# Kernel optimization log

Measured on AMD Instinct MI355X. Metric: run time of the kernel, lower is better.

The kernel has to match this reference:

```python
import jax, jax.numpy as jnp
import numpy as np
from jax import lax

B, T, E = 256, 128, 768      # batch, seq_len, bert emb dim
HE = 256                     # encoder lstm hidden (per direction)
H = 512                      # decoder hidden = 2*HE
SLOT, INTENT = 120, 64
EMB = SLOT // 3              # 40
V = SLOT + 1                 # 121, bos id = SLOT
DIN = EMB + 2 * H            # 1064 decoder lstm input
NEG = -1e12


def lstm_cell(x, h, c, Wih, Whh, bih, bhh):
    # torch gate order: i, f, g, o
    g = x @ Wih.T + h @ Whh.T + (bih + bhh)
    i, f, gg, o = jnp.split(g, 4, axis=-1)
    c = jax.nn.sigmoid(f) * c + jax.nn.sigmoid(i) * jnp.tanh(gg)
    h = jax.nn.sigmoid(o) * jnp.tanh(c)
    return h, c


def setup_inputs() -> dict:
    key = jax.random.key(0)
    ks = jax.random.split(key, 24)
    s = 0.05
    n = lambda k, shp: jax.random.normal(k, shp, jnp.float32) * s
    return {
        'seq_reps': jax.random.normal(ks[0], (B, T, E), jnp.float32),
        'nwp_index': jax.random.randint(ks[1], (B, T, 1), 0, 2),
        'slot_output_mask': jax.random.randint(ks[2], (B, T), 0, 2).astype(bool),
        'emb_table': jax.random.uniform(ks[3], (V, EMB), jnp.float32, -0.1, 0.1),
        # encoder fwd / bwd LSTM
        'Wf_ih': n(ks[4], (4 * HE, E)), 'Wf_hh': n(ks[5], (4 * HE, HE)),
        'bf_ih': n(ks[6], (4 * HE,)), 'bf_hh': n(ks[7], (4 * HE,)),
        'Wb_ih': n(ks[8], (4 * HE, E)), 'Wb_hh': n(ks[9], (4 * HE, HE)),
        'bb_ih': n(ks[10], (4 * HE,)), 'bb_hh': n(ks[11], (4 * HE,)),
        # decoder LSTM
        'Wd_ih': n(ks[12], (4 * H, DIN)), 'Wd_hh': n(ks[13], (4 * H, H)),
        'bd_ih': n(ks[14], (4 * H,)), 'bd_hh': n(ks[15], (4 * H,)),
        # attention + output heads
        'attn_W': n(ks[16], (H, H)), 'attn_b': n(ks[17], (H,)),
        'slot_W': n(ks[18], (SLOT, 2 * H)), 'slot_b': n(ks[19], (SLOT,)),
        'intent_W': n(ks[20], (INTENT, 2 * H)), 'intent_b': n(ks[21], (INTENT,)),
    }


def forward(seq_reps, nwp_index, slot_output_mask, emb_table,
            Wf_ih, Wf_hh, bf_ih, bf_hh, Wb_ih, Wb_hh, bb_ih, bb_hh,
            Wd_ih, Wd_hh, bd_ih, bd_hh, attn_W, attn_b,
            slot_W, slot_b, intent_W, intent_b):
    # ---------- Encoder: 1-layer bidirectional LSTM ----------
    xs = seq_reps.transpose(1, 0, 2)  # [T,B,E]
    z = jnp.zeros((B, HE), seq_reps.dtype)

    def fstep(carry, x):
        h, c = lstm_cell(x, carry[0], carry[1], Wf_ih, Wf_hh, bf_ih, bf_hh)
        return (h, c), h

    def bstep(carry, x):
        h, c = lstm_cell(x, carry[0], carry[1], Wb_ih, Wb_hh, bb_ih, bb_hh)
        return (h, c), h

    _, hf = lax.scan(fstep, (z, z), xs)
    _, hb = lax.scan(bstep, (z, z), xs[::-1])
    enc = jnp.concatenate([hf, hb[::-1]], -1).transpose(1, 0, 2)  # [B,T,512]

    # last real hidden: out[b, #nonzero(nwp_index[b])]
    count = jnp.clip((nwp_index[:, :, 0] != 0).sum(1), 0, T - 1)
    last_hidden = enc[jnp.arange(B), count]  # [B,H]

    # ---------- Attention (energies independent of step -> precompute) ----------
    energies = enc @ attn_W.T + attn_b  # [B,T,H]

    def attention(h):  # h: [B,H]
        e = jnp.einsum('bth,bh->bt', energies, h)
        e = jnp.where(slot_output_mask, NEG, e)
        alpha = jax.nn.softmax(e, -1)
        return jnp.einsum('bt,bth->bh', alpha, enc)  # [B,H]

    # ---------- Decoder: per-timestep LSTM + attention ----------
    bos_emb = jnp.broadcast_to(emb_table[SLOT], (B, EMB))
    zH = jnp.zeros((B, H), seq_reps.dtype)
    aligns = enc.transpose(1, 0, 2)  # [T,B,H]

    def dstep(carry, aligned):
        emb, ctx, h, c = carry
        inp = jnp.concatenate([emb, ctx, aligned], -1)  # [B,1064]
        h, c = lstm_cell(inp, h, c, Wd_ih, Wd_hh, bd_ih, bd_hh)
        score = jnp.concatenate([h, ctx], -1) @ slot_W.T + slot_b
        logp = jax.nn.log_softmax(score, -1)
        nxt = jnp.argmax(logp, -1)
        emb = emb_table[nxt]
        ctx_new = attention(h)
        return (emb, ctx_new, h, c), (logp, h, ctx_new)

    _, (logps, h_seq, ctx_seq) = lax.scan(dstep, (bos_emb, last_hidden, zH, zH), aligns)

    slot_scores = logps.transpose(1, 0, 2)  # [B,T,SLOT]
    # intent computed at step 0: intent_context == attention(h after step 0) == ctx_seq[0]
    intent_score = jnp.concatenate([h_seq[0], ctx_seq[0]], -1) @ intent_W.T + intent_b
    return slot_scores, intent_score


def reference(seq_reps, nwp_index, slot_output_mask, emb_table,
              Wf_ih, Wf_hh, bf_ih, bf_hh, Wb_ih, Wb_hh, bb_ih, bb_hh,
              Wd_ih, Wd_hh, bd_ih, bd_hh, attn_W, attn_b,
              slot_W, slot_b, intent_W, intent_b):
    return forward(seq_reps, nwp_index, slot_output_mask, emb_table,
                   Wf_ih, Wf_hh, bf_ih, bf_hh, Wb_ih, Wb_hh, bb_ih, bb_hh,
                   Wd_ih, Wd_hh, bd_ih, bd_hh, attn_W, attn_b,
                   slot_W, slot_b, intent_W, intent_b)
```

## Files before the change

### kernel.cpp

```cpp
#include <hip/hip_runtime.h>
#include <math.h>

#define Bn 256
#define Tn 128
#define En 768
#define HEn 256
#define Hn 512
#define SLOTn 120
#define INTENTn 64
#define EMBn 40
#define NEGV -1e12f

__device__ __forceinline__ float sigm(float x) { return 1.0f / (1.0f + expf(-x)); }

__global__ void zero_k(float* __restrict__ p, int n) {
    int i = blockIdx.x * blockDim.x + threadIdx.x;
    int stride = gridDim.x * blockDim.x;
    for (; i < n; i += stride) p[i] = 0.f;
}

__global__ void detect_mask_k(const unsigned char* __restrict__ m, int* __restrict__ flag) {
    __shared__ int any;
    if (threadIdx.x == 0) any = 0;
    __syncthreads();
    int found = 0;
    for (int i = threadIdx.x; i < 32768; i += 256) {
        if ((i & 3) != 0 && m[i] != 0) found = 1;
    }
    if (found) atomicOr(&any, 1);
    __syncthreads();
    if (threadIdx.x == 0) *flag = any;
}

__global__ __launch_bounds__(256) void slotwt_k(const float* __restrict__ W,
                                               float* __restrict__ wT4) {
    int idx = blockIdx.x * 256 + threadIdx.x;
    int k = idx >> 7, s = idx & 127;
    float v = (s < SLOTn) ? W[(size_t)s * 1024 + k] : 0.f;
    wT4[((size_t)(k >> 2) * 128 + s) * 4 + (k & 3)] = v;
}

__device__ __forceinline__ float4 f4zero() { float4 z; z.x = z.y = z.z = z.w = 0.f; return z; }

__device__ __forceinline__ float4 enc_wload(const float* __restrict__ Wih,
                                            const float* __restrict__ Whh,
                                            int jrow, int k) {
    return (k < En) ? *(const float4*)(Wih + (size_t)jrow * En + k)
                    : *(const float4*)(Whh + (size_t)jrow * HEn + (k - En));
}

__global__ __launch_bounds__(256) void enc_step_k(
    const float* __restrict__ seq,
    const float* __restrict__ Wf_ih, const float* __restrict__ Wf_hh,
    const float* __restrict__ bf_ih, const float* __restrict__ bf_hh,
    const float* __restrict__ Wb_ih, const float* __restrict__ Wb_hh,
    const float* __restrict__ bb_ih, const float* __restrict__ bb_hh,
    const float* __restrict__ hf_in, float* __restrict__ hf_out, float* __restrict__ cf,
    const float* __restrict__ hb_in, float* __restrict__ hb_out, float* __restrict__ cb,
    float* __restrict__ enc, int step)
{
    const int dir = blockIdx.z;
    const float* __restrict__ Wih = dir ? Wb_ih : Wf_ih;
    const float* __restrict__ Whh = dir ? Wb_hh : Wf_hh;
    const float* __restrict__ bih = dir ? bb_ih : bf_ih;
    const float* __restrict__ bhh = dir ? bb_hh : bf_hh;
    const float* __restrict__ h_in = dir ? hb_in : hf_in;
    float* __restrict__ h_out = dir ? hb_out : hf_out;
    float* __restrict__ c_st  = dir ? cb : cf;
    const int t_eff = dir ? (Tn - 1 - step) : step;

    const int jb = blockIdx.x;
    const int b0 = blockIdx.y << 5;
    const int tid = threadIdx.x;
    const int c   = tid & 63;
    const int wid = __builtin_amdgcn_readfirstlane(tid >> 6);
    const int bw  = b0 + (wid << 3);

    __shared__ float Bs[64][44];
    __shared__ float Gs[32][68];

    const int c0_ = tid >> 3,          kq0 = tid & 7;
    const int c1_ = (tid + 256) >> 3,  kq1 = tid & 7;
    const int j0row = ((c0_ >> 4) << 8) + (jb << 4) + (c0_ & 15);
    const int j1row = ((c1_ >> 4) << 8) + (jb << 4) + (c1_ & 15);

    float acc[8] = {0,0,0,0,0,0,0,0};
    float4 r0 = enc_wload(Wih, Whh, j0row, kq0 * 4);
    float4 r1 = enc_wload(Wih, Whh, j1row, kq1 * 4);

    for (int kt = 0; kt < 32; ++kt) {
        const int k0 = kt << 5;
        __syncthreads();
        *(float4*)&Bs[c0_][kq0 * 4] = r0;
        *(float4*)&Bs[c1_][kq1 * 4] = r1;
        __syncthreads();
        if (kt < 31) {
            r0 = enc_wload(Wih, Whh, j0row, k0 + 32 + kq0 * 4);
            r1 = enc_wload(Wih, Whh, j1row, k0 + 32 + kq1 * 4);
        }
#pragma unroll
        for (int g = 0; g < 8; ++g) {
            const int kk = k0 + (g << 2);
            const float* __restrict__ abase;
            size_t astr;
            if (kk < En) { abase = seq + ((size_t)bw * Tn + t_eff) * En + kk; astr = (size_t)Tn * En; }
            else         { abase = h_in + ((size_t)bw << 8) + (kk - En);      astr = HEn; }
            float4 bf = *(const float4*)&Bs[c][g << 2];
#pragma unroll
            for (int i = 0; i < 8; ++i) {
                float4 a = *(const float4*)(abase + (size_t)i * astr);
                acc[i] += a.x * bf.x + a.y * bf.y + a.z * bf.z + a.w * bf.w;
            }
        }
    }

#pragma unroll
    for (int i = 0; i < 8; ++i) Gs[(wid << 3) + i][c] = acc[i];
    __syncthreads();

#pragma unroll
    for (int r = 0; r < 2; ++r) {
        int p = tid + (r << 8);
        int row = p >> 4, jl = p & 15;
        int jg = (jb << 4) + jl;
        int b = b0 + row;
        float gi = Gs[row][jl]      + bih[jg]           + bhh[jg];
        float gf = Gs[row][16 + jl] + bih[HEn + jg]     + bhh[HEn + jg];
        float gg = Gs[row][32 + jl] + bih[2 * HEn + jg] + bhh[2 * HEn + jg];
        float go = Gs[row][48 + jl] + bih[3 * HEn + jg] + bhh[3 * HEn + jg];
        float ii = sigm(gi), ff = sigm(gf), tg = tanhf(gg), oo = sigm(go);
        int ci = (b << 8) + jg;
        float cn = ff * c_st[ci] + ii * tg;
        float hn = oo * tanhf(cn);
        c_st[ci] = cn;
        h_out[ci] = hn;
        enc[((size_t)t_eff * Bn + b) * Hn + dir * HEn + jg] = hn;
    }
}

__global__ __launch_bounds__(256) void energT_k(
    const float* __restrict__ enc, const float* __restrict__ attn_W,
    float* __restrict__ energT)
{
    const int nb = blockIdx.x;
    const int mb = blockIdx.y;
    const int t = mb >> 2, b0 = (mb & 3) << 6;
    const int tid = threadIdx.x;
    const int tx = tid & 15, ty = tid >> 4;
    __shared__ float As[32][68];
    __shared__ float Bs[32][68];
    float acc[4][4] = {};
    for (int kt = 0; kt < 16; ++kt) {
        int k0 = kt << 5;
#pragma unroll
        for (int r = 0; r < 8; ++r) {
            int idx = tid + (r << 8);
            int kk = idx & 31, row = idx >> 5;
            As[kk][row] = enc[((size_t)t * Bn + b0 + row) * Hn + k0 + kk];
            Bs[kk][row] = attn_W[(nb * 64 + row) * Hn + k0 + kk];
        }
        __syncthreads();
#pragma unroll
        for (int kk = 0; kk < 32; ++kk) {
            float a0 = As[kk][ty * 4], a1 = As[kk][ty * 4 + 1];
            float a2 = As[kk][ty * 4 + 2], a3 = As[kk][ty * 4 + 3];
            float w0 = Bs[kk][tx * 4], w1 = Bs[kk][tx * 4 + 1];
            float w2 = Bs[kk][tx * 4 + 2], w3 = Bs[kk][tx * 4 + 3];
            acc[0][0] += a0 * w0; acc[0][1] += a0 * w1; acc[0][2] += a0 * w2; acc[0][3] += a0 * w3;
            acc[1][0] += a1 * w0; acc[1][1] += a1 * w1; acc[1][2] += a1 * w2; acc[1][3] += a1 * w3;
            acc[2][0] += a2 * w0; acc[2][1] += a2 * w1; acc[2][2] += a2 * w2; acc[2][3] += a2 * w3;
            acc[3][0] += a3 * w0; acc[3][1] += a3 * w1; acc[3][2] += a3 * w2; acc[3][3] += a3 * w3;
        }
        __syncthreads();
    }
#pragma unroll
    for (int i = 0; i < 4; ++i)
#pragma unroll
        for (int q = 0; q < 4; ++q)
            energT[((size_t)(b0 + ty * 4 + i) * Hn + nb * 64 + tx * 4 + q) * Tn + t] = acc[i][q];
}

__global__ __launch_bounds__(64) void init2_k(
    const int* __restrict__ nwp, const float* __restrict__ enc,
    const float* __restrict__ emb_table,
    float* __restrict__ ctx0, float* __restrict__ embb)
{
    int b = blockIdx.x;
    int lane = threadIdx.x;
    int p1 = (nwp[b * Tn + lane] != 0);
    int p2 = (nwp[b * Tn + lane + 64] != 0);
    unsigned long long m1 = __ballot(p1), m2 = __ballot(p2);
    int cnt = __popcll(m1) + __popcll(m2);
    int idx = cnt < (Tn - 1) ? cnt : (Tn - 1);
#pragma unroll
    for (int r = 0; r < 8; ++r) {
        int j = lane + (r << 6);
        ctx0[(b << 9) + j] = enc[((size_t)idx * Bn + b) * Hn + j];
    }
    if (lane < EMBn) embb[b * EMBn + lane] = emb_table[SLOTn * EMBn + lane];
}

__device__ __forceinline__ float4 dec_wload(const float* __restrict__ Wih,
                                            const float* __restrict__ Whh,
                                            int jrow, int k) {
    if (k < 1064) return *(const float4*)(Wih + (size_t)jrow * 1064 + k);
    if (k < 1576) return *(const float4*)(Whh + ((size_t)jrow << 9) + (k - 1064));
    return f4zero();
}

__global__ __launch_bounds__(256) void dec_step_k(
    const float* __restrict__ embb, const float* __restrict__ ctx_in,
    const float* __restrict__ enc, const float* __restrict__ h_in,
    float* __restrict__ h_out, float* __restrict__ c_st,
    const float* __restrict__ Wih, const float* __restrict__ Whh,
    const float* __restrict__ bih, const float* __restrict__ bhh,
    float* __restrict__ h0_out, int step)
{
    const int jb = blockIdx.x;
    const int b0 = blockIdx.y << 5;
    const int tid = threadIdx.x;
    const int c   = tid & 63;
    const int wid = __builtin_amdgcn_readfirstlane(tid >> 6);
    const int bw  = b0 + (wid << 3);

    __shared__ float Bs[64][44];
    __shared__ float Gs[32][68];

    const int c0_ = tid >> 3,          kq0 = tid & 7;
    const int c1_ = (tid + 256) >> 3,  kq1 = tid & 7;
    const int j0row = ((c0_ >> 4) << 9) + (jb << 4) + (c0_ & 15);
    const int j1row = ((c1_ >> 4) << 9) + (jb << 4) + (c1_ & 15);

    float acc[8] = {0,0,0,0,0,0,0,0};
    float4 r0 = dec_wload(Wih, Whh, j0row, kq0 * 4);
    float4 r1 = dec_wload(Wih, Whh, j1row, kq1 * 4);

    for (int kt = 0; kt < 50; ++kt) {
        const int k0 = kt << 5;
        __syncthreads();
        *(float4*)&Bs[c0_][kq0 * 4] = r0;
        *(float4*)&Bs[c1_][kq1 * 4] = r1;
        __syncthreads();
        if (kt < 49) {
            r0 = dec_wload(Wih, Whh, j0row, k0 + 32 + kq0 * 4);
            r1 = dec_wload(Wih, Whh, j1row, k0 + 32 + kq1 * 4);
        }
#pragma unroll
        for (int g = 0; g < 8; ++g) {
            const int kk = k0 + (g << 2);
            if (kk < 1576) {
                const float* __restrict__ abase;
                size_t astr;
                if (kk < 40)        { abase = embb   + (size_t)bw * EMBn + kk;               astr = EMBn; }
                else if (kk < 552)  { abase = ctx_in + ((size_t)bw << 9) + (kk - 40);        astr = Hn; }
                else if (kk < 1064) { abase = enc + ((size_t)step * Bn + bw) * Hn + (kk - 552); astr = Hn; }
                else                { abase = h_in  + ((size_t)bw << 9) + (kk - 1064);       astr = Hn; }
                float4 bf = *(const float4*)&Bs[c][g << 2];
#pragma unroll
                for (int i = 0; i < 8; ++i) {
                    float4 a = *(const float4*)(abase + (size_t)i * astr);
                    acc[i] += a.x * bf.x + a.y * bf.y + a.z * bf.z + a.w * bf.w;
                }
            }
        }
    }

#pragma unroll
    for (int i = 0; i < 8; ++i) Gs[(wid << 3) + i][c] = acc[i];
    __syncthreads();

#pragma unroll
    for (int r = 0; r < 2; ++r) {
        int p = tid + (r << 8);
        int row = p >> 4, jl = p & 15;
        int jg = (jb << 4) + jl;
        int b = b0 + row;
        float gi = Gs[row][jl]      + bih[jg]          + bhh[jg];
        float gf = Gs[row][16 + jl] + bih[Hn + jg]     + bhh[Hn + jg];
        float gg = Gs[row][32 + jl] + bih[2 * Hn + jg] + bhh[2 * Hn + jg];
        float go = Gs[row][48 + jl] + bih[3 * Hn + jg] + bhh[3 * Hn + jg];
        float ii = sigm(gi), ff = sigm(gf), tg = tanhf(gg), oo = sigm(go);
        int ci = (b << 9) + jg;
        float cn = ff * c_st[ci] + ii * tg;
        float hn = oo * tanhf(cn);
        c_st[ci] = cn;
        h_out[ci] = hn;
        if (h0_out) h0_out[ci] = hn;
    }
}

__global__ __launch_bounds__(256) void dec_attn_slot_k(
    const float* __restrict__ enc, const float* __restrict__ energT,
    const float* __restrict__ h, const float* __restrict__ ctx_in,
    float* __restrict__ ctx_out, const unsigned char* __restrict__ mask_u8,
    const int* __restrict__ mask_i32, const int* __restrict__ mask_flag,
    const float* __restrict__ wT4, const float* __restrict__ slot_b,
    const float* __restrict__ emb_table, float* __restrict__ embb,
    float* __restrict__ out_slot, float* __restrict__ ctx0_save, int step)
{
    __shared__ float hs[512];
    __shared__ float red2[8][132];
    __shared__ float es[128];
    __shared__ float redm[2];
    __shared__ float ctxp[2][512];
    __shared__ float pacc[2][8][132];
    __shared__ float sc[8][132];
    __shared__ float logZ[8];
    __shared__ int amax[8];

    const int bid = blockIdx.x;
    const int tid = threadIdx.x;

    if (bid < Bn) {
        const int b = bid;
        hs[tid] = h[(b << 9) + tid];
        hs[tid + 256] = h[(b << 9) + 256 + tid];
        __syncthreads();
        {
            const int tg = tid & 31, jg = tid >> 5;
            const float* __restrict__ ep = energT + ((size_t)b * Hn + jg * 64) * Tn + (tg << 2);
            float4 a = f4zero();
#pragma unroll 8
            for (int jj = 0; jj < 64; ++jj) {
                float hv = hs[jg * 64 + jj];
                float4 e4 = *(const float4*)(ep + (size_t)jj * Tn);
                a.x += e4.x * hv; a.y += e4.y * hv; a.z += e4.z * hv; a.w += e4.w * hv;
            }
            *(float4*)&red2[jg][tg << 2] = a;
        }
        __syncthreads();
        if (tid < 128) {
            float e = 0.f;
#pragma unroll
            for (int jg = 0; jg < 8; ++jg) e += red2[jg][tid];
            bool mv = (*mask_flag) ? (mask_u8[(size_t)b * Tn + tid] != 0)
                                   : (mask_i32[(size_t)b * Tn + tid] != 0);
            es[tid] = mv ? NEGV : e;
        }
        __syncthreads();
        if (tid < 64) {
            float v = fmaxf(es[tid], es[tid + 64]);
            for (int o = 32; o; o >>= 1) v = fmaxf(v, __shfl_down(v, o));
            if (tid == 0) redm[0] = v;
        }
        __syncthreads();
        float m = redm[0];
        if (tid < 128) es[tid] = __expf(es[tid] - m);
        __syncthreads();
        if (tid < 64) {
            float v = es[tid] + es[tid + 64];
            for (int o = 32; o; o >>= 1) v += __shfl_down(v, o);
            if (tid == 0) redm[0] = v;
        }
        __syncthreads();
        float inv = 1.0f / redm[0];
        if (tid < 128) es[tid] *= inv;
        __syncthreads();
        {
            const int dq = tid & 127, th = tid >> 7;
            const int d = dq << 2;
            const float* __restrict__ ep2 = enc + (b << 9) + d;
            float4 a = f4zero();
            const int tbase = th << 6;
#pragma unroll 8
            for (int t2 = 0; t2 < 64; ++t2) {
                float al = es[tbase + t2];
                float4 e4 = *(const float4*)(ep2 + (size_t)(tbase + t2) * (Bn * Hn));
                a.x += al * e4.x; a.y += al * e4.y; a.z += al * e4.z; a.w += al * e4.w;
            }
            *(float4*)&ctxp[th][d] = a;
        }
        __syncthreads();
        {
            float v0 = ctxp[0][tid] + ctxp[1][tid];
            float v1 = ctxp[0][tid + 256] + ctxp[1][tid + 256];
            ctx_out[(b << 9) + tid] = v0;
            ctx_out[(b << 9) + 256 + tid] = v1;
            if (ctx0_save) {
                ctx0_save[(b << 9) + tid] = v0;
                ctx0_save[(b << 9) + 256 + tid] = v1;
            }
        }
    } else {
        const int b_base = (bid - Bn) << 3;
        const int sl = tid & 127;
        const int kg = __builtin_amdgcn_readfirstlane(tid >> 7);
        const float* __restrict__ a0 = (kg ? ctx_in : h) + ((size_t)b_base << 9);
        const float* __restrict__ wb = wT4 + (size_t)kg * 128 * 128 * 4;
        float acc[8] = {0,0,0,0,0,0,0,0};
        for (int k4 = 0; k4 < 128; ++k4) {
            const int k = k4 << 2;
            float4 w4 = *(const float4*)(wb + ((size_t)k4 * 128 + sl) * 4);
#pragma unroll
            for (int i = 0; i < 8; ++i) {
                const float* __restrict__ ar = a0 + ((size_t)i << 9) + k;
                acc[i] += w4.x * ar[0] + w4.y * ar[1] + w4.z * ar[2] + w4.w * ar[3];
            }
        }
#pragma unroll
        for (int i = 0; i < 8; ++i) pacc[kg][i][sl] = acc[i];
        __syncthreads();
        if (tid < 128) {
            float sb = (tid < SLOTn) ? slot_b[tid] : 0.f;
#pragma unroll
            for (int i = 0; i < 8; ++i)
                sc[i][tid] = pacc[0][i][tid] + pacc[1][i][tid] + sb;
        }
        __syncthreads();
        if (tid < 8) {
            float mm = -INFINITY; int am = 0;
            for (int ss = 0; ss < SLOTn; ++ss) {
                float v = sc[tid][ss];
                if (v > mm) { mm = v; am = ss; }
            }
            float sum = 0.f;
            for (int ss = 0; ss < SLOTn; ++ss) sum += __expf(sc[tid][ss] - mm);
            logZ[tid] = mm + logf(sum);
            amax[tid] = am;
        }
        __syncthreads();
        for (int r = 0; r < 4; ++r) {
            int idx = tid + (r << 8);
            int bl = idx >> 7, ss = idx & 127;
            if (ss < SLOTn)
                out_slot[(size_t)(b_base + bl) * Tn * SLOTn + step * SLOTn + ss] =
                    sc[bl][ss] - logZ[bl];
        }
        for (int i = tid; i < 8 * EMBn; i += 256) {
            int bl = i / EMBn, e2 = i % EMBn;
            embb[(b_base + bl) * EMBn + e2] = emb_table[amax[bl] * EMBn + e2];
        }
    }
}

__global__ __launch_bounds__(256) void intent_k(
    const float* __restrict__ h0, const float* __restrict__ ctx0,
    const float* __restrict__ W, const float* __restrict__ bias,
    float* __restrict__ out)
{
    __shared__ float ins[8][1032];
    __shared__ float Ws[16][68];
    const int tid = threadIdx.x;
    const int b_base = blockIdx.x << 3;
    for (int r = 0; r < 32; ++r) {
        int idx = tid + (r << 8);
        int bl = idx >> 10, k = idx & 1023;
        int b = b_base + bl;
        ins[bl][k] = (k < 512) ? h0[(b << 9) + k] : ctx0[(b << 9) + (k - 512)];
    }
    __syncthreads();
    const int n = tid & 63, bq = tid >> 6;
    float acc0 = 0.f, acc1 = 0.f;
    for (int kt = 0; kt < 64; ++kt) {
        int k0 = kt << 4;
#pragma unroll
        for (int r = 0; r < 4; ++r) {
            int idx = tid + (r << 8);
            int kk = idx & 15, nn = idx >> 4;
            Ws[kk][nn] = W[nn * 1024 + k0 + kk];
        }
        __syncthreads();
#pragma unroll
        for (int kk = 0; kk < 16; ++kk) {
            float w = Ws[kk][n];
            acc0 += w * ins[bq * 2][k0 + kk];
            acc1 += w * ins[bq * 2 + 1][k0 + kk];
        }
        __syncthreads();
    }
    out[(b_base + bq * 2) * INTENTn + n] = acc0 + bias[n];
    out[(b_base + bq * 2 + 1) * INTENTn + n] = acc1 + bias[n];
}

extern "C" void kernel_launch(void* const* d_in, const int* in_sizes, int n_in,
                              void* d_out, int out_size, void* d_ws, size_t ws_size,
                              hipStream_t stream) {
    (void)in_sizes; (void)n_in; (void)out_size; (void)ws_size;

    const float* seq      = (const float*)d_in[0];
    const int*   nwp      = (const int*)d_in[1];
    const unsigned char* mask_u8 = (const unsigned char*)d_in[2];
    const int*   mask_i32 = (const int*)d_in[2];
    const float* embt     = (const float*)d_in[3];
    const float* Wf_ih    = (const float*)d_in[4];
    const float* Wf_hh    = (const float*)d_in[5];
    const float* bf_ih    = (const float*)d_in[6];
    const float* bf_hh    = (const float*)d_in[7];
    const float* Wb_ih    = (const float*)d_in[8];
    const float* Wb_hh    = (const float*)d_in[9];
    const float* bb_ih    = (const float*)d_in[10];
    const float* bb_hh    = (const float*)d_in[11];
    const float* Wd_ih    = (const float*)d_in[12];
    const float* Wd_hh    = (const float*)d_in[13];
    const float* bd_ih    = (const float*)d_in[14];
    const float* bd_hh    = (const float*)d_in[15];
    const float* attn_W   = (const float*)d_in[16];
    const float* slot_W   = (const float*)d_in[18];
    const float* slot_b   = (const float*)d_in[19];
    const float* intent_W = (const float*)d_in[20];
    const float* intent_b = (const float*)d_in[21];

    float* Wp = (float*)d_ws;
    size_t off = 0;
    float* enc    = Wp + off; off += (size_t)Tn * Bn * Hn;
    float* energT = Wp + off; off += (size_t)Bn * Hn * Tn;
    float* zbase  = Wp + off;
    float* hf0 = Wp + off; off += Bn * HEn;
    float* hf1 = Wp + off; off += Bn * HEn;
    float* cf  = Wp + off; off += Bn * HEn;
    float* hb0 = Wp + off; off += Bn * HEn;
    float* hb1 = Wp + off; off += Bn * HEn;
    float* cb  = Wp + off; off += Bn * HEn;
    float* hd0 = Wp + off; off += Bn * Hn;
    float* hd1 = Wp + off; off += Bn * Hn;
    float* cd  = Wp + off; off += Bn * Hn;
    int nzero = (int)(Wp + off - zbase);
    float* ctx0b = Wp + off; off += Bn * Hn;
    float* ctx1b = Wp + off; off += Bn * Hn;
    float* h0s   = Wp + off; off += Bn * Hn;
    float* ctx0s = Wp + off; off += Bn * Hn;
    float* embb  = Wp + off; off += Bn * EMBn;
    int* mask_flag = (int*)(Wp + off); off += 1;
    float* wT4   = Wp + off; off += 1024 * 128;

    float* out = (float*)d_out;

    zero_k<<<512, 256, 0, stream>>>(zbase, nzero);
    detect_mask_k<<<1, 256, 0, stream>>>(mask_u8, mask_flag);
    slotwt_k<<<512, 256, 0, stream>>>(slot_W, wT4);

    for (int s = 0; s < Tn; ++s) {
        const float* hinf = (s & 1) ? hf1 : hf0;
        float* houtf      = (s & 1) ? hf0 : hf1;
        const float* hinb = (s & 1) ? hb1 : hb0;
        float* houtb      = (s & 1) ? hb0 : hb1;
        enc_step_k<<<dim3(16, 8, 2), 256, 0, stream>>>(
            seq, Wf_ih, Wf_hh, bf_ih, bf_hh, Wb_ih, Wb_hh, bb_ih, bb_hh,
            hinf, houtf, cf, hinb, houtb, cb, enc, s);
    }

    energT_k<<<dim3(8, 512), 256, 0, stream>>>(enc, attn_W, energT);
    init2_k<<<256, 64, 0, stream>>>(nwp, enc, embt, ctx0b, embb);

    for (int t = 0; t < Tn; ++t) {
        const float* ctxin = (t & 1) ? ctx1b : ctx0b;
        float* ctxout      = (t & 1) ? ctx0b : ctx1b;
        const float* hin   = (t & 1) ? hd1 : hd0;
        float* hout        = (t & 1) ? hd0 : hd1;
        dec_step_k<<<dim3(32, 8), 256, 0, stream>>>(
            embb, ctxin, enc, hin, hout, cd,
            Wd_ih, Wd_hh, bd_ih, bd_hh, (t == 0) ? h0s : (float*)nullptr, t);
        dec_attn_slot_k<<<288, 256, 0, stream>>>(
            enc, energT, hout, ctxin, ctxout, mask_u8, mask_i32, mask_flag,
            wT4, slot_b, embt, embb, out, (t == 0) ? ctx0s : (float*)nullptr, t);
    }

    intent_k<<<32, 256, 0, stream>>>(h0s, ctx0s, intent_W, intent_b,
                                     out + (size_t)Bn * Tn * SLOTn);
}
```

Measured before the change: 47.51 ms.

## Double-buffer weight tiles and use 512-thread blocks in LSTM step kernels

```diff
diff --git a/kernel.cpp b/kernel.cpp
--- a/kernel.cpp
+++ b/kernel.cpp
@@ -49,7 +49,7 @@
                     : *(const float4*)(Whh + (size_t)jrow * HEn + (k - En));
 }
 
-__global__ __launch_bounds__(256) void enc_step_k(
+__global__ __launch_bounds__(512) void enc_step_k(
     const float* __restrict__ seq,
     const float* __restrict__ Wf_ih, const float* __restrict__ Wf_hh,
     const float* __restrict__ bf_ih, const float* __restrict__ bf_hh,
@@ -74,54 +74,58 @@
     const int tid = threadIdx.x;
     const int c   = tid & 63;
     const int wid = __builtin_amdgcn_readfirstlane(tid >> 6);
-    const int bw  = b0 + (wid << 3);
-
-    __shared__ float Bs[64][44];
+    const int bw  = b0 + (wid << 2);
+
+    __shared__ float Bs[2][64][68];
     __shared__ float Gs[32][68];
 
-    const int c0_ = tid >> 3,          kq0 = tid & 7;
-    const int c1_ = (tid + 256) >> 3,  kq1 = tid & 7;
-    const int j0row = ((c0_ >> 4) << 8) + (jb << 4) + (c0_ & 15);
-    const int j1row = ((c1_ >> 4) << 8) + (jb << 4) + (c1_ & 15);
-
-    float acc[8] = {0,0,0,0,0,0,0,0};
-    float4 r0 = enc_wload(Wih, Whh, j0row, kq0 * 4);
-    float4 r1 = enc_wload(Wih, Whh, j1row, kq1 * 4);
-
-    for (int kt = 0; kt < 32; ++kt) {
-        const int k0 = kt << 5;
-        __syncthreads();
-        *(float4*)&Bs[c0_][kq0 * 4] = r0;
-        *(float4*)&Bs[c1_][kq1 * 4] = r1;
-        __syncthreads();
-        if (kt < 31) {
-            r0 = enc_wload(Wih, Whh, j0row, k0 + 32 + kq0 * 4);
-            r1 = enc_wload(Wih, Whh, j1row, k0 + 32 + kq1 * 4);
-        }
-#pragma unroll
-        for (int g = 0; g < 8; ++g) {
+    const int cs0 = tid >> 4,          kq0 = tid & 15;
+    const int cs1 = (tid + 512) >> 4;
+    const int j0row = ((cs0 >> 4) << 8) + (jb << 4) + (cs0 & 15);
+    const int j1row = ((cs1 >> 4) << 8) + (jb << 4) + (cs1 & 15);
+
+    float acc[4] = {0,0,0,0};
+
+    float4 p0 = enc_wload(Wih, Whh, j0row, kq0 << 2);
+    float4 p1 = enc_wload(Wih, Whh, j1row, kq0 << 2);
+    *(float4*)&Bs[0][cs0][kq0 << 2] = p0;
+    *(float4*)&Bs[0][cs1][kq0 << 2] = p1;
+    __syncthreads();
+
+    for (int t = 0; t < 16; ++t) {
+        const int k0 = t << 6;
+        const int buf = t & 1;
+        if (t < 15) {
+            p0 = enc_wload(Wih, Whh, j0row, k0 + 64 + (kq0 << 2));
+            p1 = enc_wload(Wih, Whh, j1row, k0 + 64 + (kq0 << 2));
+        }
+#pragma unroll
+        for (int g = 0; g < 16; ++g) {
             const int kk = k0 + (g << 2);
             const float* __restrict__ abase;
             size_t astr;
             if (kk < En) { abase = seq + ((size_t)bw * Tn + t_eff) * En + kk; astr = (size_t)Tn * En; }
             else         { abase = h_in + ((size_t)bw << 8) + (kk - En);      astr = HEn; }
-            float4 bf = *(const float4*)&Bs[c][g << 2];
-#pragma unroll
-            for (int i = 0; i < 8; ++i) {
+            float4 bf = *(const float4*)&Bs[buf][c][g << 2];
+#pragma unroll
+            for (int i = 0; i < 4; ++i) {
                 float4 a = *(const float4*)(abase + (size_t)i * astr);
                 acc[i] += a.x * bf.x + a.y * bf.y + a.z * bf.z + a.w * bf.w;
             }
         }
-    }
-
-#pragma unroll
-    for (int i = 0; i < 8; ++i) Gs[(wid << 3) + i][c] = acc[i];
-    __syncthreads();
-
-#pragma unroll
-    for (int r = 0; r < 2; ++r) {
-        int p = tid + (r << 8);
-        int row = p >> 4, jl = p & 15;
+        if (t < 15) {
+            *(float4*)&Bs[buf ^ 1][cs0][kq0 << 2] = p0;
+            *(float4*)&Bs[buf ^ 1][cs1][kq0 << 2] = p1;
+        }
+        __syncthreads();
+    }
+
+#pragma unroll
+    for (int i = 0; i < 4; ++i) Gs[(wid << 2) + i][c] = acc[i];
+    __syncthreads();
+
+    {
+        int row = tid >> 4, jl = tid & 15;
         int jg = (jb << 4) + jl;
         int b = b0 + row;
         float gi = Gs[row][jl]      + bih[jg]           + bhh[jg];
@@ -208,7 +212,7 @@
     return f4zero();
 }
 
-__global__ __launch_bounds__(256) void dec_step_k(
+__global__ __launch_bounds__(512) void dec_step_k(
     const float* __restrict__ embb, const float* __restrict__ ctx_in,
     const float* __restrict__ enc, const float* __restrict__ h_in,
     float* __restrict__ h_out, float* __restrict__ c_st,
@@ -221,32 +225,33 @@
     const int tid = threadIdx.x;
     const int c   = tid & 63;
     const int wid = __builtin_amdgcn_readfirstlane(tid >> 6);
-    const int bw  = b0 + (wid << 3);
-
-    __shared__ float Bs[64][44];
+    const int bw  = b0 + (wid << 2);
+
+    __shared__ float Bs[2][64][68];
     __shared__ float Gs[32][68];
 
-    const int c0_ = tid >> 3,          kq0 = tid & 7;
-    const int c1_ = (tid + 256) >> 3,  kq1 = tid & 7;
-    const int j0row = ((c0_ >> 4) << 9) + (jb << 4) + (c0_ & 15);
-    const int j1row = ((c1_ >> 4) << 9) + (jb << 4) + (c1_ & 15);
-
-    float acc[8] = {0,0,0,0,0,0,0,0};
-    float4 r0 = dec_wload(Wih, Whh, j0row, kq0 * 4);
-    float4 r1 = dec_wload(Wih, Whh, j1row, kq1 * 4);
-
-    for (int kt = 0; kt < 50; ++kt) {
-        const int k0 = kt << 5;
-        __syncthreads();
-        *(float4*)&Bs[c0_][kq0 * 4] = r0;
-        *(float4*)&Bs[c1_][kq1 * 4] = r1;
-        __syncthreads();
-        if (kt < 49) {
-            r0 = dec_wload(Wih, Whh, j0row, k0 + 32 + kq0 * 4);
-            r1 = dec_wload(Wih, Whh, j1row, k0 + 32 + kq1 * 4);
-        }
-#pragma unroll
-        for (int g = 0; g < 8; ++g) {
+    const int cs0 = tid >> 4,          kq0 = tid & 15;
+    const int cs1 = (tid + 512) >> 4;
+    const int j0row = ((cs0 >> 4) << 9) + (jb << 4) + (cs0 & 15);
+    const int j1row = ((cs1 >> 4) << 9) + (jb << 4) + (cs1 & 15);
+
+    float acc[4] = {0,0,0,0};
+
+    float4 p0 = dec_wload(Wih, Whh, j0row, kq0 << 2);
+    float4 p1 = dec_wload(Wih, Whh, j1row, kq0 << 2);
+    *(float4*)&Bs[0][cs0][kq0 << 2] = p0;
+    *(float4*)&Bs[0][cs1][kq0 << 2] = p1;
+    __syncthreads();
+
+    for (int t = 0; t < 25; ++t) {
+        const int k0 = t << 6;
+        const int buf = t & 1;
+        if (t < 24) {
+            p0 = dec_wload(Wih, Whh, j0row, k0 + 64 + (kq0 << 2));
+            p1 = dec_wload(Wih, Whh, j1row, k0 + 64 + (kq0 << 2));
+        }
+#pragma unroll
+        for (int g = 0; g < 16; ++g) {
             const int kk = k0 + (g << 2);
             if (kk < 1576) {
                 const float* __restrict__ abase;
@@ -255,24 +260,27 @@
                 else if (kk < 552)  { abase = ctx_in + ((size_t)bw << 9) + (kk - 40);        astr = Hn; }
                 else if (kk < 1064) { abase = enc + ((size_t)step * Bn + bw) * Hn + (kk - 552); astr = Hn; }
                 else                { abase = h_in  + ((size_t)bw << 9) + (kk - 1064);       astr = Hn; }
-                float4 bf = *(const float4*)&Bs[c][g << 2];
-#pragma unroll
-                for (int i = 0; i < 8; ++i) {
+                float4 bf = *(const float4*)&Bs[buf][c][g << 2];
+#pragma unroll
+                for (int i = 0; i < 4; ++i) {
                     float4 a = *(const float4*)(abase + (size_t)i * astr);
                     acc[i] += a.x * bf.x + a.y * bf.y + a.z * bf.z + a.w * bf.w;
                 }
             }
         }
-    }
-
-#pragma unroll
-    for (int i = 0; i < 8; ++i) Gs[(wid << 3) + i][c] = acc[i];
-    __syncthreads();
-
-#pragma unroll
-    for (int r = 0; r < 2; ++r) {
-        int p = tid + (r << 8);
-        int row = p >> 4, jl = p & 15;
+        if (t < 24) {
+            *(float4*)&Bs[buf ^ 1][cs0][kq0 << 2] = p0;
+            *(float4*)&Bs[buf ^ 1][cs1][kq0 << 2] = p1;
+        }
+        __syncthreads();
+    }
+
+#pragma unroll
+    for (int i = 0; i < 4; ++i) Gs[(wid << 2) + i][c] = acc[i];
+    __syncthreads();
+
+    {
+        int row = tid >> 4, jl = tid & 15;
         int jg = (jb << 4) + jl;
         int b = b0 + row;
         float gi = Gs[row][jl]      + bih[jg]          + bhh[jg];
@@ -534,7 +542,7 @@
         float* houtf      = (s & 1) ? hf0 : hf1;
         const float* hinb = (s & 1) ? hb1 : hb0;
         float* houtb      = (s & 1) ? hb0 : hb1;
-        enc_step_k<<<dim3(16, 8, 2), 256, 0, stream>>>(
+        enc_step_k<<<dim3(16, 8, 2), 512, 0, stream>>>(
             seq, Wf_ih, Wf_hh, bf_ih, bf_hh, Wb_ih, Wb_hh, bb_ih, bb_hh,
             hinf, houtf, cf, hinb, houtb, cb, enc, s);
     }
@@ -547,7 +555,7 @@
         float* ctxout      = (t & 1) ? ctx0b : ctx1b;
         const float* hin   = (t & 1) ? hd1 : hd0;
         float* hout        = (t & 1) ? hd0 : hd1;
-        dec_step_k<<<dim3(32, 8), 256, 0, stream>>>(
+        dec_step_k<<<dim3(32, 8), 512, 0, stream>>>(
             embb, ctxin, enc, hin, hout, cd,
             Wd_ih, Wd_hh, bd_ih, bd_hh, (t == 0) ? h0s : (float*)nullptr, t);
         dec_attn_slot_k<<<288, 256, 0, stream>>>(
```

New measurement: 48.63 ms. 1.02x slower.
